# Kernel tuning notes

Hardware: AMD Instinct MI355X
Metric: run time of the kernel (lower is better)

Reference implementation:

```python
import jax, jax.numpy as jnp
import numpy as np

INF = 1e5
EPS = 1e-8
B, NRES, NRIG = 1, 448, 512
C_S, C_Z, C_H, H, PQ, PV = 384, 128, 16, 12, 4, 8


def _quat_to_rot(q):
    q = q / jnp.linalg.norm(q, axis=-1, keepdims=True)
    w, x, y, z = q[..., 0], q[..., 1], q[..., 2], q[..., 3]
    return jnp.stack([
        jnp.stack([1 - 2 * (y * y + z * z), 2 * (x * y - w * z), 2 * (x * z + w * y)], -1),
        jnp.stack([2 * (x * y + w * z), 1 - 2 * (x * x + z * z), 2 * (y * z - w * x)], -1),
        jnp.stack([2 * (x * z - w * y), 2 * (y * z + w * x), 1 - 2 * (x * x + y * y)], -1),
    ], -2)


def setup_inputs() -> dict:
    key = jax.random.key(0)
    ks = jax.random.split(key, 16)
    lin = lambda k, i, o: (jax.random.normal(k, (i, o), jnp.float32) / np.sqrt(i))
    hc = H * C_H
    return dict(
        s=jax.random.normal(ks[0], (B, NRIG, C_S), jnp.float32),
        z=jax.random.normal(ks[1], (B, NRES, NRES, C_Z), jnp.float32),
        rot=_quat_to_rot(jax.random.normal(ks[2], (B, NRIG, 4), jnp.float32)),
        trans=jax.random.normal(ks[3], (B, NRIG, 3), jnp.float32) * 10.0,
        mask=jnp.ones((B, NRIG), jnp.float32),
        rigid_to_res_idx=jax.random.randint(ks[4], (B, NRIG), 0, NRES),
        w_q=lin(ks[5], C_S, hc), b_q=jnp.zeros((hc,), jnp.float32),
        w_kv=lin(ks[6], C_S, 2 * hc), b_kv=jnp.zeros((2 * hc,), jnp.float32),
        w_qp=lin(ks[7], C_S, H * PQ * 3), b_qp=jnp.zeros((H * PQ * 3,), jnp.float32),
        w_kvp=lin(ks[8], C_S, H * (PQ + PV) * 3), b_kvp=jnp.zeros((H * (PQ + PV) * 3,), jnp.float32),
        w_b=lin(ks[9], C_Z, H), b_b=jnp.zeros((H,), jnp.float32),
        w_dz=lin(ks[10], C_Z, C_Z // 4), b_dz=jnp.zeros((C_Z // 4,), jnp.float32),
        head_weights=jnp.full((H,), 0.5413, jnp.float32),  # softplus^-1(1)
        w_out=lin(ks[11], H * (C_Z // 4 + C_H + PV * 4), C_S),
        b_out=jnp.zeros((C_S,), jnp.float32),
    )


def _fwd(s, z, rot, trans, mask, rigid_to_res_idx,
         w_q, b_q, w_kv, b_kv, w_qp, b_qp, w_kvp, b_kvp,
         w_b, b_b, w_dz, b_dz, head_weights, w_out, b_out):
    Bd, nr, _ = s.shape
    nres = z.shape[-2]
    h = w_b.shape[-1]
    ch = w_q.shape[-1] // h
    pq = w_qp.shape[-1] // (3 * h)
    pkv = w_kvp.shape[-1] // (3 * h)
    pv = pkv - pq

    q = (s @ w_q + b_q).reshape(Bd, nr, h, ch)
    kv = (s @ w_kv + b_kv).reshape(Bd, nr, h, 2 * ch)
    k, v = kv[..., :ch], kv[..., ch:]

    def to_pts(flat):
        # flat: [B,nr,3*D] laid out as 3 coordinate chunks -> global-frame pts [B,nr,D,3]
        D = flat.shape[-1] // 3
        p = jnp.moveaxis(flat.reshape(Bd, nr, 3, D), -2, -1)
        return jnp.einsum('bnij,bndj->bndi', rot, p) + trans[:, :, None, :]

    q_pts = to_pts(s @ w_qp + b_qp).reshape(Bd, nr, h, pq, 3)
    kv_pts = to_pts(s @ w_kvp + b_kvp).reshape(Bd, nr, h, pkv, 3)
    k_pts, v_pts = kv_pts[..., :pq, :], kv_pts[..., pq:, :]

    # pair bias gathered rigid->res on both axes
    bi = jnp.arange(Bd)[:, None, None]
    b_pair = z @ w_b + b_b  # [B,Nres,Nres,H]
    b_bcast = b_pair[bi, rigid_to_res_idx[:, :, None], rigid_to_res_idx[:, None, :]]  # [B,nr,nr,H]

    a = jnp.einsum('bihc,bjhc->bhij', q, k) * np.sqrt(1.0 / (3 * ch))
    a = a + np.sqrt(1.0 / 3) * jnp.moveaxis(b_bcast, -1, -3)

    # squared-distance point attention
    diff = q_pts[:, :, None] - k_pts[:, None]  # [B,nr,nr,h,pq,3]
    sq = jnp.sum(diff * diff, -1)              # [B,nr,nr,h,pq]
    hw = jax.nn.softplus(head_weights) * np.sqrt(1.0 / (3 * (pq * 9.0 / 2)))
    pt_att = -0.5 * jnp.sum(sq * hw[:, None], -1)  # [B,nr,nr,h]
    a = a + jnp.moveaxis(pt_att, -1, -3)

    sq_mask = INF * (mask[:, :, None] * mask[:, None, :] - 1.0)
    a = jax.nn.softmax(a + sq_mask[:, None], axis=-1)  # [B,h,nr,nr]

    o = jnp.einsum('bhij,bjhc->bihc', a, v).reshape(Bd, nr, h * ch)

    o_pt_g = jnp.einsum('bhij,bjhpx->bihpx', a, v_pts)  # [B,nr,h,pv,3]
    o_pt = jnp.einsum('bnji,bnhpj->bnhpi', rot, o_pt_g - trans[:, :, None, None, :])  # invert_apply
    o_pt_norm = jnp.sqrt(jnp.sum(o_pt * o_pt, -1) + EPS).reshape(Bd, nr, h * pv)
    o_pt = o_pt.reshape(Bd, nr, h * pv, 3)

    pair_z = z @ w_dz + b_dz  # [B,Nres,Nres,cz4]
    pz_rig = pair_z[jnp.arange(Bd)[:, None], rigid_to_res_idx]  # [B,nr,Nres,cz4]
    # faithful to the torch scatter_add_: the index varies over the QUERY rigid i
    # (constant over keys j), so row i's full softmax mass lands in column res(i).
    onehot = jax.nn.one_hot(rigid_to_res_idx, nres, dtype=a.dtype)  # [B,nr,Nres]
    a_agg = a.sum(-1)[..., None] * onehot[:, None]  # [B,h,nr,Nres]
    o_pair = jnp.einsum('bhin,bind->bihd', a_agg, pz_rig).reshape(Bd, nr, -1)

    feats = jnp.concatenate([o, o_pt[..., 0], o_pt[..., 1], o_pt[..., 2], o_pt_norm, o_pair], -1)
    return feats @ w_out + b_out


def reference(s, z, rot, trans, mask, rigid_to_res_idx, w_q, b_q, w_kv, b_kv, w_qp, b_qp, w_kvp, b_kvp, w_b, b_b, w_dz, b_dz, head_weights, w_out, b_out):
    return _fwd(s, z, rot, trans, mask, rigid_to_res_idx, w_q, b_q, w_kv, b_kv, w_qp, b_qp, w_kvp, b_kvp, w_b, b_b, w_dz, b_dz, head_weights, w_out, b_out)
```

## Files before the change

### kernel.cpp

```cpp
#include <hip/hip_runtime.h>
#include <hip/hip_bf16.h>
#include <math.h>

constexpr int NRIG = 512;
constexpr int NRES = 448;
constexpr int CS   = 384;
constexpr int CZ   = 128;
constexpr int CH   = 16;
constexpr int NH   = 12;
constexpr int PQ   = 4;
constexpr int PV   = 8;
constexpr int HC   = NH * CH;
constexpr int NPAIR = NRES*NRES;
constexpr float INF_ = 100000.0f;
constexpr float SC_ = 0.57735026918962584f;

constexpr size_t OFF_Q   = 0;
constexpr size_t OFF_KT  = OFF_Q   + (size_t)NH*NRIG*16;
constexpr size_t OFF_QP  = OFF_KT  + (size_t)NH*16*NRIG;
constexpr size_t OFF_KPT = OFF_QP  + (size_t)NH*NRIG*12;
constexpr size_t OFF_VT  = OFF_KPT + (size_t)NH*12*NRIG;
constexpr size_t OFF_O   = OFF_VT  + (size_t)NH*40*NRIG;
constexpr size_t OFF_OPT = OFF_O   + (size_t)NRIG*HC;
constexpr size_t OFF_RS  = OFF_OPT + (size_t)NRIG*NH*PV*3;
constexpr size_t OFF_BP  = OFF_RS  + (size_t)NRIG*NH;
constexpr size_t OFF_RAW = OFF_BP  + (size_t)NH*NPAIR;
constexpr size_t OFF_F   = OFF_RAW + (size_t)NRIG*576;
constexpr size_t OFF_P3  = OFF_F   + (size_t)NRIG*960;

constexpr int ZWB_BLOCKS = NPAIR/128;

__global__ __launch_bounds__(256) void prep_kernel(
    const float* __restrict__ z,  const float* __restrict__ wb, const float* __restrict__ bb,
    const float* __restrict__ s,
    const float* __restrict__ wq,  const float* __restrict__ bq,
    const float* __restrict__ wkv, const float* __restrict__ bkv,
    const float* __restrict__ wqp, const float* __restrict__ bqp,
    const float* __restrict__ wkvp,const float* __restrict__ bkvp,
    float* __restrict__ ws)
{
    __shared__ float smem[18560];
    const int t = threadIdx.x;

    if ((int)blockIdx.x < ZWB_BLOCKS) {
        float* sZ   = smem;
        float* sRed = smem + 16896;
        const size_t r0 = (size_t)blockIdx.x * 128;
        #pragma unroll
        for (int k = 0; k < 16; ++k) {
            int i = k*256 + t;
            int row = i >> 5, c4 = i & 31;
            float4 f = *(const float4*)(z + (r0+row)*CZ + (c4<<2));
            *(float4*)&sZ[row*132 + ((c4 ^ (row&7))<<2)] = f;
        }
        __syncthreads();
        const int wid = t >> 6, lane = t & 63;
        const int rB = ((wid>>1)<<6) | lane;
        const int ch = wid & 1;
        float acc[12] = {0,0,0,0,0,0,0,0,0,0,0,0};
        const int cb = ch*16;
        #pragma unroll
        for (int i = 0; i < 16; ++i) {
            const int c4 = cb + i;
            float4 zf = *(const float4*)&sZ[rB*132 + ((c4 ^ (rB&7))<<2)];
            #pragma unroll
            for (int e = 0; e < 4; ++e) {
                const float zv = (&zf.x)[e];
                const float* wr = wb + (c4*4+e)*12;
                #pragma unroll
                for (int h = 0; h < 12; ++h) acc[h] += zv * wr[h];
            }
        }
        if (ch == 0) {
            #pragma unroll
            for (int h = 0; h < 12; ++h) sRed[rB*13 + h] = acc[h];
        }
        __syncthreads();
        if (ch == 1) {
            float* bp = ws + OFF_BP;
            #pragma unroll
            for (int h = 0; h < 12; ++h) {
                float v = (acc[h] + sRed[rB*13 + h] + bb[h]) * SC_;
                bp[(size_t)h*NPAIR + r0 + rB] = v;
            }
        }
    } else {
        constexpr int BM=64, BN=32, BK=32, LDA=68;
        float (*sA)[LDA] = (float(*)[LDA])smem;
        float (*sB)[BN]  = (float(*)[BN])(smem + 2176);
        const int bid = (int)blockIdx.x - ZWB_BLOCKS;
        const int m0 = (bid & 7) * BM;
        const int c0 = (bid >> 3) * BN;
        const int tx = t & 15, ty = t >> 4;

        float acc[4][2] = {};
        for (int kt = 0; kt < CS/BK; ++kt) {
            const int k0 = kt*BK;
            #pragma unroll
            for (int r = 0; r < 2; ++r) {
                int qd = r*256 + t;
                int m = qd >> 3, kq = (qd & 7) << 2;
                float4 f = *(const float4*)(s + (size_t)(m0+m)*CS + k0 + kq);
                sA[kq+0][m] = f.x; sA[kq+1][m] = f.y;
                sA[kq+2][m] = f.z; sA[kq+3][m] = f.w;
            }
            {
                int kk = t >> 3, c4 = (t & 7) << 2;
                int c = c0 + c4;
                const float* wp; int ld, co;
                if (c < 192)      { wp = wq;   ld = 192; co = c;     }
                else if (c < 576) { wp = wkv;  ld = 384; co = c-192; }
                else if (c < 720) { wp = wqp;  ld = 144; co = c-576; }
                else              { wp = wkvp; ld = 432; co = c-720; }
                float4 f = *(const float4*)(wp + (size_t)(k0+kk)*ld + co);
                *(float4*)&sB[kk][c4] = f;
            }
            __syncthreads();
            #pragma unroll
            for (int kk = 0; kk < BK; ++kk) {
                float4 a = *(const float4*)&sA[kk][ty*4];
                float2 b = *(const float2*)&sB[kk][tx*2];
                acc[0][0] += a.x*b.x; acc[0][1] += a.x*b.y;
                acc[1][0] += a.y*b.x; acc[1][1] += a.y*b.y;
                acc[2][0] += a.z*b.x; acc[2][1] += a.z*b.y;
                acc[3][0] += a.w*b.x; acc[3][1] += a.w*b.y;
            }
            __syncthreads();
        }
        float* qw  = ws + OFF_Q;  float* ktw = ws + OFF_KT;  float* vt = ws + OFF_VT;
        float* raw = ws + OFF_RAW;
        #pragma unroll
        for (int i = 0; i < 4; ++i)
            #pragma unroll
            for (int j = 0; j < 2; ++j) {
                int n = m0 + ty*4 + i;
                int c = c0 + tx*2 + j;
                if (c < 192) {
                    int hh = c >> 4, cc = c & 15;
                    qw[((size_t)hh*NRIG + n)*16 + cc] = acc[i][j] + bq[c];
                } else if (c < 576) {
                    int e = c-192; float val = acc[i][j] + bkv[e];
                    int hh = e >> 5, sub = e & 31;
                    if (sub < CH) ktw[((size_t)hh*16 + sub)*NRIG + n] = val;
                    else          vt [((size_t)hh*40 + (sub-CH))*NRIG + n] = val;
                } else {
                    int e = c-576;
                    float bb_ = (c < 720) ? bqp[e] : bkvp[c-720];
                    raw[(size_t)n*576 + e] = acc[i][j] + bb_;
                }
            }
    }
}

__global__ __launch_bounds__(256) void rotate_kernel(
    const float* __restrict__ rot, const float* __restrict__ trans,
    const float* __restrict__ raw_in, float* __restrict__ qpw,
    float* __restrict__ kptw, float* __restrict__ vtw)
{
    const int gid = blockIdx.x*256 + threadIdx.x;
    const int n = gid / 192, d = gid % 192;
    const float* raw = raw_in + (size_t)n*576;
    float px, py, pzz;
    if (d < 48) { px = raw[d];      py = raw[48+d];       pzz = raw[96+d]; }
    else { int dd = d-48; px = raw[144+dd]; py = raw[288+dd]; pzz = raw[432+dd]; }
    const float* R = rot   + (size_t)n*9;
    const float* T = trans + (size_t)n*3;
    float gx = R[0]*px + R[1]*py + R[2]*pzz + T[0];
    float gy = R[3]*px + R[4]*py + R[5]*pzz + T[1];
    float gz = R[6]*px + R[7]*py + R[8]*pzz + T[2];
    if (d < 48) {
        int hh = d >> 2, pp = d & 3;
        float* dst = qpw + ((size_t)hh*NRIG + n)*12 + pp*3;
        dst[0]=gx; dst[1]=gy; dst[2]=gz;
    } else {
        int dd = d-48; int hh = dd/12, pp = dd%12;
        if (pp < PQ) {
            float* kpt = kptw + (size_t)hh*12*NRIG;
            kpt[(size_t)(pp*3+0)*NRIG + n] = gx;
            kpt[(size_t)(pp*3+1)*NRIG + n] = gy;
            kpt[(size_t)(pp*3+2)*NRIG + n] = gz;
        } else {
            float* vt = vtw + ((size_t)hh*40 + 16 + (pp-PQ)*3)*NRIG + n;
            vt[0*NRIG]=gx; vt[1*NRIG]=gy; vt[2*NRIG]=gz;
        }
    }
}

__global__ __launch_bounds__(256) void attn_kernel(
    const float* __restrict__ hw_in, const float* __restrict__ mask,
    const int* __restrict__ ridx,
    const float* __restrict__ qw_all,  const float* __restrict__ ktw_all,
    const float* __restrict__ qpw_all, const float* __restrict__ kpt_all,
    const float* __restrict__ vt_all,  const float* __restrict__ bp_all,
    float* __restrict__ o_out, float* __restrict__ opt_out, float* __restrict__ rs_out)
{
    constexpr int TI = 8;
    const int h    = blockIdx.x;
    const int i0   = blockIdx.y * TI;
    const int t    = threadIdx.x;
    const int lane = t & 63, wid = t >> 6;

    __shared__ float sE[TI*516];
    __shared__ float sP[16][TI][45];
    __shared__ float sS[TI];

    const float* qw  = qw_all  + (size_t)h*NRIG*16;
    const float* ktw = ktw_all + (size_t)h*16*NRIG;
    const float* qpw = qpw_all + (size_t)h*NRIG*12;
    const float* kpt = kpt_all + (size_t)h*12*NRIG;
    const float* vt  = vt_all  + (size_t)h*40*NRIG;
    const float* bph = bp_all  + (size_t)h*NPAIR;

    const float hwv = -0.5f * log1pf(__expf(hw_in[h])) * 0.13608276348795434f;
    const float QKS = 0.14433756729740643f;

    #pragma unroll
    for (int jj = 0; jj < 2; ++jj) {
        const int j = t + jj*256;
        float kk[16], kpv[12];
        #pragma unroll
        for (int c = 0; c < 16; ++c) kk[c]  = ktw[c*NRIG + j];
        #pragma unroll
        for (int e = 0; e < 12; ++e) kpv[e] = kpt[e*NRIG + j];
        const float mj = mask[j];
        const int   rj = ridx[j];
        #pragma unroll
        for (int qq = 0; qq < TI; ++qq) {
            const float* qv  = qw  + (size_t)(i0+qq)*16;
            const float* qpv = qpw + (size_t)(i0+qq)*12;
            const float  mi  = mask[i0+qq];
            const int    ri  = ridx[i0+qq];
            float dot = 0.f;
            #pragma unroll
            for (int c = 0; c < 16; ++c) dot += qv[c]*kk[c];
            float sq = 0.f;
            #pragma unroll
            for (int e = 0; e < 12; ++e) { float d = qpv[e]-kpv[e]; sq += d*d; }
            const float bv = bph[(size_t)ri*NRES + rj];
            const float lgt = dot*QKS + bv + hwv*sq + INF_*(mi*mj - 1.0f);
            sE[qq*516 + j] = __expf(lgt);
        }
    }
    __syncthreads();

    {
        float acc[11][TI];
        #pragma unroll
        for (int ci=0;ci<11;++ci)
            #pragma unroll
            for (int qq=0;qq<TI;++qq) acc[ci][qq]=0.f;

        #pragma unroll
        for (int m = 0; m < 8; ++m) {
            const int j = lane + (m<<6);
            float ev[TI];
            #pragma unroll
            for (int qq=0;qq<TI;++qq) ev[qq] = sE[qq*516 + j];
            #pragma unroll
            for (int ci = 0; ci < 11; ++ci) {
                if (ci < 10 || wid == 0) {
                    const int c = wid + (ci<<2);
                    const float vv = (c == 40) ? 1.0f : vt[(size_t)c*NRIG + j];
                    #pragma unroll
                    for (int qq=0;qq<TI;++qq) acc[ci][qq] += ev[qq]*vv;
                }
            }
        }
        #pragma unroll
        for (int ci=0;ci<11;++ci)
            if (ci < 10 || wid == 0)
                #pragma unroll
                for (int qq=0;qq<TI;++qq) {
                    acc[ci][qq] += __shfl_xor(acc[ci][qq], 1);
                    acc[ci][qq] += __shfl_xor(acc[ci][qq], 2);
                }
        if ((lane & 3) == 0) {
            const int g = lane >> 2;
            #pragma unroll
            for (int ci=0;ci<11;++ci)
                if (ci < 10 || wid == 0) {
                    const int c = wid + (ci<<2);
                    #pragma unroll
                    for (int qq=0;qq<TI;++qq) sP[g][qq][c] = acc[ci][qq];
                }
        }
    }
    __syncthreads();

    if (t < TI) {
        float S = 0.f;
        #pragma unroll
        for (int g = 0; g < 16; ++g) S += sP[g][t][40];
        sS[t] = S;
    }
    __syncthreads();

    for (int e = t; e < TI*41; e += 256) {
        const int qq = e / 41, c = e % 41;
        const int n = i0 + qq;
        float sum = 0.f;
        #pragma unroll
        for (int g = 0; g < 16; ++g) sum += sP[g][qq][c];
        const float val = sum * (1.0f / sS[qq]);
        if (c < 16)       o_out[((size_t)n*NH + h)*CH + c]        = val;
        else if (c < 40)  opt_out[((size_t)n*NH + h)*24 + (c-16)] = val;
        else              rs_out[(size_t)n*NH + h]                = val;
    }
}

__global__ __launch_bounds__(256) void feats_kernel(
    const float* __restrict__ rot, const float* __restrict__ trans,
    const float* __restrict__ z, const int* __restrict__ ridx,
    const float* __restrict__ wdz, const float* __restrict__ bdz,
    const float* __restrict__ o_ws, const float* __restrict__ optg,
    const float* __restrict__ rs, float* __restrict__ F)
{
    constexpr int TI = 4;
    __shared__ float sZd[TI][CZ];
    __shared__ float sPz[TI][32];
    const int i0 = blockIdx.x*TI;
    const int t  = threadIdx.x;

    for (int e = t; e < TI*CZ; e += 256) {
        int qq = e >> 7, c = e & 127;
        int ri = ridx[i0+qq];
        sZd[qq][c] = z[((size_t)ri*NRES + ri)*CZ + c];
    }
    for (int e = t; e < TI*HC; e += 256) {
        int qq = e/HC, c = e%HC;
        F[(size_t)(i0+qq)*960 + c] = o_ws[(size_t)(i0+qq)*HC + c];
    }
    for (int e = t; e < TI*96; e += 256) {
        int qq = e/96, hp = e%96; int n = i0+qq;
        const float* g = optg + ((size_t)n*NH + hp/PV)*24 + (hp%PV)*3;
        float gx = g[0]-trans[n*3+0], gy = g[1]-trans[n*3+1], gz = g[2]-trans[n*3+2];
        const float* R = rot + (size_t)n*9;
        float lx = R[0]*gx + R[3]*gy + R[6]*gz;
        float ly = R[1]*gx + R[4]*gy + R[7]*gz;
        float lz = R[2]*gx + R[5]*gy + R[8]*gz;
        float* Fr = F + (size_t)n*960;
        Fr[192+hp] = lx; Fr[288+hp] = ly; Fr[384+hp] = lz;
        Fr[480+hp] = sqrtf(lx*lx+ly*ly+lz*lz + 1e-8f);
    }
    __syncthreads();
    if (t < TI*32) {
        int qq = t >> 5, d = t & 31;
        float acc = 0.f;
        #pragma unroll 8
        for (int c = 0; c < CZ; ++c) acc += sZd[qq][c] * wdz[(size_t)c*32 + d];
        sPz[qq][d] = acc + bdz[d];
    }
    __syncthreads();
    for (int e = t; e < TI*384; e += 256) {
        int qq = e/384, hd = e%384; int n = i0+qq;
        F[(size_t)n*960 + 576 + hd] = rs[(size_t)n*NH + (hd>>5)] * sPz[qq][hd&31];
    }
}

__global__ __launch_bounds__(256) void out_gemm_kernel(
    const float* __restrict__ w_out, const float* __restrict__ F,
    float* __restrict__ P)
{
    constexpr int BM=64, BN=32, BK=32, LDA=68;
    __shared__ float sA[BK][LDA];
    __shared__ float sB[BK][BN];
    const int m0 = blockIdx.x * BM;
    const int c0 = blockIdx.y * BN;
    const int ks = blockIdx.z;
    const int t  = threadIdx.x;
    const int tx = t & 15, ty = t >> 4;

    float acc[4][2] = {};
    for (int kt = 0; kt < 10; ++kt) {
        const int k0 = ks*320 + kt*BK;
        #pragma unroll
        for (int r = 0; r < 2; ++r) {
            int qd = r*256 + t;
            int m = qd >> 3, kq = (qd & 7) << 2;
            float4 f = *(const float4*)(F + (size_t)(m0+m)*960 + k0 + kq);
            sA[kq+0][m] = f.x; sA[kq+1][m] = f.y;
            sA[kq+2][m] = f.z; sA[kq+3][m] = f.w;
        }
        {
            int kk = t >> 3, c4 = (t & 7) << 2;
            float4 f = *(const float4*)(w_out + (size_t)(k0+kk)*CS + c0 + c4);
            *(float4*)&sB[kk][c4] = f;
        }
        __syncthreads();
        #pragma unroll
        for (int kk = 0; kk < BK; ++kk) {
            float4 a = *(const float4*)&sA[kk][ty*4];
            float2 b = *(const float2*)&sB[kk][tx*2];
            acc[0][0] += a.x*b.x; acc[0][1] += a.x*b.y;
            acc[1][0] += a.y*b.x; acc[1][1] += a.y*b.y;
            acc[2][0] += a.z*b.x; acc[2][1] += a.z*b.y;
            acc[3][0] += a.w*b.x; acc[3][1] += a.w*b.y;
        }
        __syncthreads();
    }
    #pragma unroll
    for (int i = 0; i < 4; ++i)
        #pragma unroll
        for (int j = 0; j < 2; ++j) {
            int n = m0 + ty*4 + i;
            int c = c0 + tx*2 + j;
            P[(size_t)ks*NRIG*CS + (size_t)n*CS + c] = acc[i][j];
        }
}

__global__ __launch_bounds__(256) void reduce_kernel(
    const float* __restrict__ P, const float* __restrict__ b_out,
    float* __restrict__ out)
{
    const int i4 = blockIdx.x*256 + threadIdx.x;
    const size_t base = (size_t)i4 * 4;
    float4 a = *(const float4*)(P + base);
    float4 b = *(const float4*)(P + (size_t)NRIG*CS + base);
    float4 c = *(const float4*)(P + (size_t)2*NRIG*CS + base);
    const int cc = (int)(base % CS);
    float4 bv = *(const float4*)(b_out + cc);
    float4 r;
    r.x = a.x+b.x+c.x+bv.x; r.y = a.y+b.y+c.y+bv.y;
    r.z = a.z+b.z+c.z+bv.z; r.w = a.w+b.w+c.w+bv.w;
    *(float4*)(out + base) = r;
}

extern "C" void kernel_launch(void* const* d_in, const int* in_sizes, int n_in,
                              void* d_out, int out_size, void* d_ws, size_t ws_size,
                              hipStream_t stream)
{
    const float* s     = (const float*)d_in[0];
    const float* z     = (const float*)d_in[1];
    const float* rot   = (const float*)d_in[2];
    const float* trans = (const float*)d_in[3];
    const float* mask  = (const float*)d_in[4];
    const int*   ridx  = (const int*)  d_in[5];
    const float* wq    = (const float*)d_in[6];
    const float* bq    = (const float*)d_in[7];
    const float* wkv   = (const float*)d_in[8];
    const float* bkv   = (const float*)d_in[9];
    const float* wqp   = (const float*)d_in[10];
    const float* bqp   = (const float*)d_in[11];
    const float* wkvp  = (const float*)d_in[12];
    const float* bkvp  = (const float*)d_in[13];
    const float* wb    = (const float*)d_in[14];
    const float* bb    = (const float*)d_in[15];
    const float* wdz   = (const float*)d_in[16];
    const float* bdz   = (const float*)d_in[17];
    const float* hw    = (const float*)d_in[18];
    const float* wout  = (const float*)d_in[19];
    const float* bout  = (const float*)d_in[20];
    float* ws  = (float*)d_ws;
    float* out = (float*)d_out;

    hipLaunchKernelGGL(prep_kernel, dim3(ZWB_BLOCKS + 288), dim3(256), 0, stream,
        z, wb, bb, s, wq,bq, wkv,bkv, wqp,bqp, wkvp,bkvp, ws);
    hipLaunchKernelGGL(rotate_kernel, dim3(NRIG*192/256), dim3(256), 0, stream,
        rot, trans, ws+OFF_RAW, ws+OFF_QP, ws+OFF_KPT, ws+OFF_VT);
    hipLaunchKernelGGL(attn_kernel, dim3(NH, NRIG/8), dim3(256), 0, stream,
        hw, mask, ridx, ws+OFF_Q, ws+OFF_KT, ws+OFF_QP, ws+OFF_KPT,
        ws+OFF_VT, ws+OFF_BP, ws+OFF_O, ws+OFF_OPT, ws+OFF_RS);
    hipLaunchKernelGGL(feats_kernel, dim3(NRIG/4), dim3(256), 0, stream,
        rot, trans, z, ridx, wdz, bdz, ws+OFF_O, ws+OFF_OPT, ws+OFF_RS, ws+OFF_F);
    hipLaunchKernelGGL(out_gemm_kernel, dim3(NRIG/64, CS/32, 3), dim3(256), 0, stream,
        wout, ws+OFF_F, ws+OFF_P3);
    hipLaunchKernelGGL(reduce_kernel, dim3(NRIG*CS/4/256), dim3(256), 0, stream,
        ws+OFF_P3, bout, out);
}
```

Before: 125.2 us.

## Restructure z·w_b projection: 256 rows per block, transposed LDS, chunked K loop

```diff
diff --git a/kernel.cpp b/kernel.cpp
--- a/kernel.cpp
+++ b/kernel.cpp
@@ -28,7 +28,7 @@
 constexpr size_t OFF_F   = OFF_RAW + (size_t)NRIG*576;
 constexpr size_t OFF_P3  = OFF_F   + (size_t)NRIG*960;
 
-constexpr int ZWB_BLOCKS = NPAIR/128;
+constexpr int ZWB_BLOCKS = NPAIR/256;
 
 __global__ __launch_bounds__(256) void prep_kernel(
     const float* __restrict__ z,  const float* __restrict__ wb, const float* __restrict__ bb,
@@ -39,51 +39,41 @@
     const float* __restrict__ wkvp,const float* __restrict__ bkvp,
     float* __restrict__ ws)
 {
-    __shared__ float smem[18560];
+    __shared__ float smem[8224];
     const int t = threadIdx.x;
 
     if ((int)blockIdx.x < ZWB_BLOCKS) {
-        float* sZ   = smem;
-        float* sRed = smem + 16896;
-        const size_t r0 = (size_t)blockIdx.x * 128;
-        #pragma unroll
-        for (int k = 0; k < 16; ++k) {
-            int i = k*256 + t;
-            int row = i >> 5, c4 = i & 31;
-            float4 f = *(const float4*)(z + (r0+row)*CZ + (c4<<2));
-            *(float4*)&sZ[row*132 + ((c4 ^ (row&7))<<2)] = f;
-        }
-        __syncthreads();
-        const int wid = t >> 6, lane = t & 63;
-        const int rB = ((wid>>1)<<6) | lane;
-        const int ch = wid & 1;
+        float (*sZt)[257] = (float(*)[257])smem;
+        const size_t r0 = (size_t)blockIdx.x * 256;
         float acc[12] = {0,0,0,0,0,0,0,0,0,0,0,0};
-        const int cb = ch*16;
-        #pragma unroll
-        for (int i = 0; i < 16; ++i) {
-            const int c4 = cb + i;
-            float4 zf = *(const float4*)&sZ[rB*132 + ((c4 ^ (rB&7))<<2)];
-            #pragma unroll
-            for (int e = 0; e < 4; ++e) {
-                const float zv = (&zf.x)[e];
-                const float* wr = wb + (c4*4+e)*12;
-                #pragma unroll
-                for (int h = 0; h < 12; ++h) acc[h] += zv * wr[h];
-            }
-        }
-        if (ch == 0) {
-            #pragma unroll
-            for (int h = 0; h < 12; ++h) sRed[rB*13 + h] = acc[h];
-        }
-        __syncthreads();
-        if (ch == 1) {
-            float* bp = ws + OFF_BP;
-            #pragma unroll
-            for (int h = 0; h < 12; ++h) {
-                float v = (acc[h] + sRed[rB*13 + h] + bb[h]) * SC_;
-                bp[(size_t)h*NPAIR + r0 + rB] = v;
-            }
-        }
+
+        for (int kc = 0; kc < 4; ++kc) {
+            if (kc) __syncthreads();
+            #pragma unroll
+            for (int k = 0; k < 8; ++k) {
+                const int i = k*256 + t;
+                const int row = i >> 3, c4 = i & 7;
+                float4 f = *(const float4*)(z + (r0+row)*CZ + kc*32 + (c4<<2));
+                sZt[c4*4+0][row] = f.x;
+                sZt[c4*4+1][row] = f.y;
+                sZt[c4*4+2][row] = f.z;
+                sZt[c4*4+3][row] = f.w;
+            }
+            __syncthreads();
+            #pragma unroll 8
+            for (int c = 0; c < 32; ++c) {
+                const float zv = sZt[c][t];
+                const float4* wr4 = (const float4*)(wb + (size_t)(kc*32+c)*12);
+                const float4 w0 = wr4[0], w1 = wr4[1], w2 = wr4[2];
+                acc[0] += zv*w0.x; acc[1] += zv*w0.y; acc[2]  += zv*w0.z; acc[3]  += zv*w0.w;
+                acc[4] += zv*w1.x; acc[5] += zv*w1.y; acc[6]  += zv*w1.z; acc[7]  += zv*w1.w;
+                acc[8] += zv*w2.x; acc[9] += zv*w2.y; acc[10] += zv*w2.z; acc[11] += zv*w2.w;
+            }
+        }
+        float* bp = ws + OFF_BP;
+        #pragma unroll
+        for (int h = 0; h < 12; ++h)
+            bp[(size_t)h*NPAIR + r0 + t] = (acc[h] + bb[h]) * SC_;
     } else {
         constexpr int BM=64, BN=32, BK=32, LDA=68;
         float (*sA)[LDA] = (float(*)[LDA])smem;
```

Measured after the change: 108.9 us. 1.15x faster.

## Compute z·w_b bias with register-resident weights and shuffle reductions, no LDS staging

Applied to the files above, without the earlier changes.

```diff
diff --git a/kernel.cpp b/kernel.cpp
--- a/kernel.cpp
+++ b/kernel.cpp
@@ -39,49 +39,57 @@
     const float* __restrict__ wkvp,const float* __restrict__ bkvp,
     float* __restrict__ ws)
 {
-    __shared__ float smem[18560];
+    __shared__ float smem[3200];
     const int t = threadIdx.x;
 
     if ((int)blockIdx.x < ZWB_BLOCKS) {
-        float* sZ   = smem;
-        float* sRed = smem + 16896;
+        const int lane = t & 63;
+        const int wid  = t >> 6;
+        const int hh   = wid & 1;
+        const int rgrp = wid >> 1;
+        const int kbase = (lane & 7) * 16;
         const size_t r0 = (size_t)blockIdx.x * 128;
-        #pragma unroll
-        for (int k = 0; k < 16; ++k) {
-            int i = k*256 + t;
-            int row = i >> 5, c4 = i & 31;
-            float4 f = *(const float4*)(z + (r0+row)*CZ + (c4<<2));
-            *(float4*)&sZ[row*132 + ((c4 ^ (row&7))<<2)] = f;
-        }
-        __syncthreads();
-        const int wid = t >> 6, lane = t & 63;
-        const int rB = ((wid>>1)<<6) | lane;
-        const int ch = wid & 1;
-        float acc[12] = {0,0,0,0,0,0,0,0,0,0,0,0};
-        const int cb = ch*16;
-        #pragma unroll
-        for (int i = 0; i < 16; ++i) {
-            const int c4 = cb + i;
-            float4 zf = *(const float4*)&sZ[rB*132 + ((c4 ^ (rB&7))<<2)];
-            #pragma unroll
-            for (int e = 0; e < 4; ++e) {
-                const float zv = (&zf.x)[e];
-                const float* wr = wb + (c4*4+e)*12;
+
+        float wv[16][6];
+        #pragma unroll
+        for (int kk = 0; kk < 16; ++kk)
+            #pragma unroll
+            for (int j = 0; j < 6; ++j)
+                wv[kk][j] = wb[(size_t)(kbase + kk)*12 + hh*6 + j];
+
+        float bbv[6];
+        #pragma unroll
+        for (int j = 0; j < 6; ++j) bbv[j] = bb[hh*6 + j];
+
+        float* bp = ws + OFF_BP + (size_t)hh*6*NPAIR;
+
+        for (int p = 0; p < 8; ++p) {
+            const int oct = rgrp + 2*p;
+            const size_t rowbase = r0 + (size_t)oct*8;
+            const float4* zp = (const float4*)(z + (rowbase + (lane>>3))*CZ + kbase);
+
+            float4 z0 = zp[0], z1 = zp[1], z2 = zp[2], z3 = zp[3];
+
+            float acc[6] = {0.f,0.f,0.f,0.f,0.f,0.f};
+            const float zr[16] = {z0.x,z0.y,z0.z,z0.w, z1.x,z1.y,z1.z,z1.w,
+                                  z2.x,z2.y,z2.z,z2.w, z3.x,z3.y,z3.z,z3.w};
+            #pragma unroll
+            for (int kk = 0; kk < 16; ++kk) {
+                const float zv = zr[kk];
                 #pragma unroll
-                for (int h = 0; h < 12; ++h) acc[h] += zv * wr[h];
-            }
-        }
-        if (ch == 0) {
-            #pragma unroll
-            for (int h = 0; h < 12; ++h) sRed[rB*13 + h] = acc[h];
-        }
-        __syncthreads();
-        if (ch == 1) {
-            float* bp = ws + OFF_BP;
-            #pragma unroll
-            for (int h = 0; h < 12; ++h) {
-                float v = (acc[h] + sRed[rB*13 + h] + bb[h]) * SC_;
-                bp[(size_t)h*NPAIR + r0 + rB] = v;
+                for (int j = 0; j < 6; ++j) acc[j] += zv * wv[kk][j];
+            }
+            #pragma unroll
+            for (int j = 0; j < 6; ++j) {
+                acc[j] += __shfl_xor(acc[j], 1);
+                acc[j] += __shfl_xor(acc[j], 2);
+                acc[j] += __shfl_xor(acc[j], 4);
+            }
+            if ((lane & 7) == 0) {
+                const size_t r = rowbase + (lane>>3);
+                #pragma unroll
+                for (int j = 0; j < 6; ++j)
+                    bp[(size_t)j*NPAIR + r] = (acc[j] + bbv[j]) * SC_;
             }
         }
     } else {
```

New measurement: 126.8 us. No clear change (+1.3%).
